# Kernel tuning notes

Hardware: AMD Instinct MI355X
Metric: run time of the kernel (lower is better)

The kernel has to match this reference:

```python
import jax, jax.numpy as jnp
import numpy as np

DIM = 2048
NUM_HEADS = 16
HEAD_DIM = DIM // NUM_HEADS
ROPE_BASE = 10000.0


def _rope_cache(seq_len):
    inv_freq = 1.0 / (ROPE_BASE ** (jnp.arange(0, HEAD_DIM, 2, dtype=jnp.float32) / HEAD_DIM))
    t = jnp.arange(seq_len, dtype=jnp.float32)
    freqs = jnp.einsum('i,j->ij', t, inv_freq)          # [S, HEAD_DIM//2]
    emb = jnp.concatenate([freqs, freqs], axis=-1)       # [S, HEAD_DIM]
    return jnp.cos(emb), jnp.sin(emb)


def _rotate_half(x):
    x1, x2 = jnp.split(x, 2, axis=-1)
    return jnp.concatenate([-x2, x1], axis=-1)


def setup_inputs() -> dict:
    key = jax.random.key(0)
    kx, kq, ko = jax.random.split(key, 3)
    B, S = 2, 2048
    x = jax.random.normal(kx, (B, S, DIM), dtype=jnp.float32)
    # torch nn.Linear(dim, 3*dim) weight has shape [3*dim, dim]; y = x @ W.T
    w_qkv = jax.random.normal(kq, (3 * DIM, DIM), dtype=jnp.float32) * (DIM ** -0.5)
    w_out = jax.random.normal(ko, (DIM, DIM), dtype=jnp.float32) * (DIM ** -0.5)
    return {"x": x, "w_qkv": w_qkv, "w_out": w_out}


def reference(x, w_qkv, w_out):
    B, S, _ = x.shape
    qkv = x @ w_qkv.T                                   # [B, S, 3*DIM]
    q, k, v = jnp.split(qkv, 3, axis=-1)
    def to_heads(t):
        return t.reshape(B, S, NUM_HEADS, HEAD_DIM).transpose(0, 2, 1, 3)  # [B, H, S, d]
    q, k, v = to_heads(q), to_heads(k), to_heads(v)

    cos, sin = _rope_cache(S)                           # [S, d]
    cos = cos[None, None, :, :]
    sin = sin[None, None, :, :]
    q = q * cos + _rotate_half(q) * sin
    k = k * cos + _rotate_half(k) * sin

    scale = HEAD_DIM ** -0.5
    scores = jnp.einsum('bhqd,bhkd->bhqk', q, k) * scale  # [B, H, S, S]
    causal = jnp.tril(jnp.ones((S, S), dtype=bool))
    scores = jnp.where(causal[None, None], scores, -jnp.inf)
    attn = jax.nn.softmax(scores, axis=-1)
    out = jnp.einsum('bhqk,bhkd->bhqd', attn, v)          # [B, H, S, d]
    out = out.transpose(0, 2, 1, 3).reshape(B, S, DIM)
    return out @ w_out.T
```

## Files before the change

### kernel.cpp

```cpp
#include <hip/hip_runtime.h>
#include <cstdint>
#include <cstddef>

#define NHEADS 16
#define HDIM   128
#define BATCH  2
#define SEQ    2048
#define DMODEL 2048
#define MTOT   (BATCH*SEQ)
#define NQKV   (3*DMODEL)
#define QBLK   64

typedef __attribute__((ext_vector_type(8))) __bf16 bf16x8;
typedef __attribute__((ext_vector_type(4))) float f32x4;
typedef __attribute__((ext_vector_type(8))) unsigned short ushort8v;

__device__ __forceinline__ unsigned short f2bf(float f){
  __bf16 h = (__bf16)f;
  return __builtin_bit_cast(unsigned short, h);
}
__device__ __forceinline__ float bf2f(unsigned short s){
  return __uint_as_float(((uint32_t)s) << 16);
}
__device__ __forceinline__ void gload_lds16(const void* src, void* lds_base){
  __builtin_amdgcn_global_load_lds((const __attribute__((address_space(1))) unsigned int*)src,
                                   (__attribute__((address_space(3))) unsigned int*)lds_base,
                                   16, 0, 0);
}

template<int CTRL>
__device__ __forceinline__ float dppmv(float x){
  return __uint_as_float((unsigned)__builtin_amdgcn_update_dpp(
      0, (int)__float_as_uint(x), CTRL, 0xF, 0xF, true));
}
__device__ __forceinline__ float rmax16(float x){
  x = fmaxf(x, dppmv<0x128>(x));
  x = fmaxf(x, dppmv<0x124>(x));
  x = fmaxf(x, dppmv<0x122>(x));
  x = fmaxf(x, dppmv<0x121>(x));
  return x;
}
__device__ __forceinline__ float rsum16(float x){
  x += dppmv<0x128>(x);
  x += dppmv<0x124>(x);
  x += dppmv<0x122>(x);
  x += dppmv<0x121>(x);
  return x;
}

__global__ void cast3_kernel(const float* __restrict__ s0, unsigned short* __restrict__ d0, int n0,
                             const float* __restrict__ s1, unsigned short* __restrict__ d1, int n1,
                             const float* __restrict__ s2, unsigned short* __restrict__ d2, int n2){
  const int stride = gridDim.x*blockDim.x*8;
  const int base = (blockIdx.x*blockDim.x + threadIdx.x)*8;
  #pragma unroll 1
  for (int a = 0; a < 3; ++a){
    const float* s = a==0 ? s0 : (a==1 ? s1 : s2);
    unsigned short* d = a==0 ? d0 : (a==1 ? d1 : d2);
    const int n = a==0 ? n0 : (a==1 ? n1 : n2);
    for (int i = base; i < n; i += stride){
      float4 x = *reinterpret_cast<const float4*>(s + i);
      float4 y = *reinterpret_cast<const float4*>(s + i + 4);
      ushort8v o;
      o[0]=f2bf(x.x); o[1]=f2bf(x.y); o[2]=f2bf(x.z); o[3]=f2bf(x.w);
      o[4]=f2bf(y.x); o[5]=f2bf(y.y); o[6]=f2bf(y.z); o[7]=f2bf(y.w);
      *reinterpret_cast<ushort8v*>(d + i) = o;
    }
  }
}

template<int MODE>
__global__ __launch_bounds__(512, 2) void gemm2(
    const unsigned short* __restrict__ A,
    const unsigned short* __restrict__ Bw,
    float* __restrict__ Cf,
    unsigned short* __restrict__ qo,
    unsigned short* __restrict__ ko,
    unsigned short* __restrict__ vo,
    int M, int N, int K)
{
  __shared__ __align__(16) unsigned short smem[49152];
  auto lds = reinterpret_cast<unsigned short (*)[3][128*64]>(smem);

  const int lane = threadIdx.x & 63;
  const int wid  = threadIdx.x >> 6;
  const int wm = wid >> 2, wn = wid & 3;
  const int hi = lane >> 4;
  const int l15 = lane & 15;

  const int nwg = gridDim.x * gridDim.y;
  const int bid = blockIdx.y * gridDim.x + blockIdx.x;
  const int swz = (bid & 7) * (nwg >> 3) + (bid >> 3);
  const int by = swz & 31;
  const int bx = swz >> 5;
  const int m0 = by * 128;
  const int n0 = bx * 256;

  const int NT = K >> 6;

  auto stage = [&](const unsigned short* base, int row0, int k0, int buf, int slot){
    const int rlo = wid << 4;
    #pragma unroll
    for (int i=0;i<2;++i){
      const int r = rlo + i*8 + (lane>>3);
      const int csrc = ((lane&7) ^ (lane>>3)) << 3;
      gload_lds16(base + (size_t)(row0 + r)*K + k0 + csrc,
                  &lds[buf][slot][(rlo + i*8)*64]);
    }
  };
  auto frag = [&](const unsigned short* h, int r, int s){
    return *reinterpret_cast<const bf16x8*>(h + r*64 + ((s ^ (r&7)) << 3));
  };

  f32x4 acc[4][4];
  #pragma unroll
  for (int i=0;i<4;++i)
    #pragma unroll
    for (int j=0;j<4;++j) acc[i][j] = (f32x4){0.f,0.f,0.f,0.f};

  stage(A,  m0,      0, 0, 0);
  stage(Bw, n0,      0, 0, 1);
  stage(Bw, n0+128,  0, 0, 2);
  if (NT > 1){
    stage(A, m0, 64, 1, 0);
    asm volatile("s_waitcnt vmcnt(2)" ::: "memory");
  } else {
    asm volatile("s_waitcnt vmcnt(0)" ::: "memory");
  }
  __builtin_amdgcn_sched_barrier(0);
  __builtin_amdgcn_s_barrier();

  bf16x8 Ar[4][2];
  bf16x8 Br[2][2];

  auto tile_body = [&](int kt, int cur){
    const int nxt = cur ^ 1;
    const unsigned short* Ah = &lds[cur][0][0];
    const unsigned short* Bh = &lds[cur][1 + (wn>>1)][0];
    const int rbase = (wn & 1) * 64;

    #pragma unroll
    for (int fm=0;fm<4;++fm)
      #pragma unroll
      for (int kk=0;kk<2;++kk)
        Ar[fm][kk] = frag(Ah, wm*64 + fm*16 + l15, kk*4 + hi);
    #pragma unroll
    for (int nf=0;nf<2;++nf)
      #pragma unroll
      for (int kk=0;kk<2;++kk)
        Br[nf][kk] = frag(Bh, rbase + nf*16 + l15, kk*4 + hi);
    if (kt+1 < NT){
      stage(Bw, n0,     (kt+1)*64, nxt, 1);
      stage(Bw, n0+128, (kt+1)*64, nxt, 2);
    }
    asm volatile("s_waitcnt lgkmcnt(8)" ::: "memory");
    __builtin_amdgcn_sched_barrier(0);
    __builtin_amdgcn_s_barrier();
    asm volatile("s_waitcnt lgkmcnt(0)" ::: "memory");
    __builtin_amdgcn_sched_barrier(0);
    __builtin_amdgcn_s_setprio(1);
    #pragma unroll
    for (int fm=0;fm<4;++fm){
      acc[fm][0] = __builtin_amdgcn_mfma_f32_16x16x32_bf16(Ar[fm][0], Br[0][0], acc[fm][0], 0,0,0);
      acc[fm][0] = __builtin_amdgcn_mfma_f32_16x16x32_bf16(Ar[fm][1], Br[0][1], acc[fm][0], 0,0,0);
      acc[fm][1] = __builtin_amdgcn_mfma_f32_16x16x32_bf16(Ar[fm][0], Br[1][0], acc[fm][1], 0,0,0);
      acc[fm][1] = __builtin_amdgcn_mfma_f32_16x16x32_bf16(Ar[fm][1], Br[1][1], acc[fm][1], 0,0,0);
    }
    __builtin_amdgcn_s_setprio(0);
    __builtin_amdgcn_sched_barrier(0);
    __builtin_amdgcn_s_barrier();

    #pragma unroll
    for (int nf=0;nf<2;++nf)
      #pragma unroll
      for (int kk=0;kk<2;++kk)
        Br[nf][kk] = frag(Bh, rbase + 32 + nf*16 + l15, kk*4 + hi);
    if (kt+2 < NT) stage(A, m0, (kt+2)*64, cur, 0);
    __builtin_amdgcn_sched_barrier(0);
    __builtin_amdgcn_s_barrier();
    asm volatile("s_waitcnt lgkmcnt(0)" ::: "memory");
    __builtin_amdgcn_sched_barrier(0);
    __builtin_amdgcn_s_setprio(1);
    #pragma unroll
    for (int fm=0;fm<4;++fm){
      acc[fm][2] = __builtin_amdgcn_mfma_f32_16x16x32_bf16(Ar[fm][0], Br[0][0], acc[fm][2], 0,0,0);
      acc[fm][2] = __builtin_amdgcn_mfma_f32_16x16x32_bf16(Ar[fm][1], Br[0][1], acc[fm][2], 0,0,0);
      acc[fm][3] = __builtin_amdgcn_mfma_f32_16x16x32_bf16(Ar[fm][0], Br[1][0], acc[fm][3], 0,0,0);
      acc[fm][3] = __builtin_amdgcn_mfma_f32_16x16x32_bf16(Ar[fm][1], Br[1][1], acc[fm][3], 0,0,0);
    }
    __builtin_amdgcn_s_setprio(0);
    if (kt+2 < NT)      asm volatile("s_waitcnt vmcnt(2)" ::: "memory");
    else if (kt+1 < NT) asm volatile("s_waitcnt vmcnt(0)" ::: "memory");
    __builtin_amdgcn_sched_barrier(0);
    __builtin_amdgcn_s_barrier();
  };

  for (int kt2 = 0; kt2 < NT; kt2 += 2){
    tile_body(kt2,     0);
    tile_body(kt2 + 1, 1);
  }

  if (MODE == 0 && (n0 >> 11) == 2){
    __builtin_amdgcn_s_barrier();
    unsigned short* trsp = smem;
    #pragma unroll
    for (int fm=0;fm<4;++fm){
      const int srow = wm*64 + fm*16 + hi*4;
      #pragma unroll
      for (int p=0;p<4;++p){
        const int dcol = wn*64 + p*16 + l15;
        f32x4 v = acc[fm][p];
        ushort4 pk;
        pk.x=f2bf(v[0]); pk.y=f2bf(v[1]); pk.z=f2bf(v[2]); pk.w=f2bf(v[3]);
        *reinterpret_cast<ushort4*>(trsp + dcol*136 + srow) = pk;
      }
    }
    __syncthreads();
    const int bb  = m0 >> 11;
    const int ss0 = m0 & 2047;
    const size_t vrow = (size_t)(bb*2048 + (n0 - 4096));
    const int t = threadIdx.x;
    #pragma unroll
    for (int it=0; it<8; ++it){
      const int dl = it*32 + (t>>4);
      const int ch = t & 15;
      ushort8v val = *reinterpret_cast<const ushort8v*>(trsp + dl*136 + ch*8);
      *reinterpret_cast<ushort8v*>(vo + (vrow + dl)*SEQ + ss0 + ch*8) = val;
    }
  } else {
    #pragma unroll
    for (int fm=0;fm<4;++fm){
      const int row0 = m0 + wm*64 + fm*16 + (hi<<2);
      #pragma unroll
      for (int p=0;p<4;++p){
        const int col = n0 + wn*64 + p*16 + l15;
        f32x4 v = acc[fm][p];
        if (MODE == 1){
          #pragma unroll
          for (int r=0;r<4;++r) Cf[(size_t)(row0+r)*N + col] = v[r];
        } else {
          const int part = col >> 11;
          const int hh = (col >> 7) & 15;
          const int d  = col & 127;
          const int bb = row0 >> 11;
          const int ss = row0 & 2047;
          unsigned short* base = (part == 0 ? qo : ko)
                               + ((size_t)(bb*NHEADS+hh)*SEQ + ss)*HDIM + d;
          #pragma unroll
          for (int r=0;r<4;++r) base[r*HDIM] = f2bf(v[r]);
        }
      }
    }
  }
}

__global__ void rope_kernel(unsigned short* __restrict__ qh, unsigned short* __restrict__ kh){
  const int idx = blockIdx.x * blockDim.x + threadIdx.x;
  const int j  = idx & 63;
  const int s  = (idx >> 6) & 2047;
  const int bh = (idx >> 17) & 31;
  const int t  = idx >> 22;
  unsigned short* base = (t ? kh : qh) + ((size_t)bh*SEQ + s)*HDIM;
  const float x1 = bf2f(base[j]);
  const float x2 = bf2f(base[j+64]);
  const float inv = exp2f(-(float)j * (13.287712379549449f/64.f));
  const float ang = (float)s * inv;
  float sn, cs;
  sincosf(ang, &sn, &cs);
  float o1 = x1*cs - x2*sn;
  float o2 = x2*cs + x1*sn;
  const float QSCALE = 0.08838834764831845f * 1.4426950408889634f;
  if (t == 0){ o1 *= QSCALE; o2 *= QSCALE; }
  base[j]    = f2bf(o1);
  base[j+64] = f2bf(o2);
}

__global__ __launch_bounds__(256, 2) void attn_kernel(
    const unsigned short* __restrict__ qh,
    const unsigned short* __restrict__ kh,
    const unsigned short* __restrict__ vT,
    unsigned short* __restrict__ ao)
{
  __shared__ __align__(16) unsigned short Ks[2][64*128];
  __shared__ __align__(16) unsigned short Vs[2][128*64];
  __shared__ __align__(16) unsigned short Ps[4][16*64];

  const int lane = threadIdx.x & 63;
  const int wid  = threadIdx.x >> 6;
  const int hi   = lane >> 4;
  const int pr = blockIdx.x;
  const int bh = blockIdx.y;
  const int b_ = bh >> 4, h_ = bh & 15;

  const unsigned short* Qb = qh + (size_t)bh * SEQ * HDIM;
  const unsigned short* Kb = kh + (size_t)bh * SEQ * HDIM;
  const unsigned short* Vb = vT + (size_t)bh * HDIM * SEQ;

  auto stageKV = [&](int kg, int buf){
    #pragma unroll
    for (int i=0;i<4;++i){
      const int r  = (wid*4+i)*4 + (lane>>4);
      const int cb = ((lane&15)<<4) ^ ((r&7)<<4);
      gload_lds16(Kb + (size_t)(kg*64 + r)*HDIM + (cb>>1), &Ks[buf][0] + (wid*4+i)*512);
    }
    #pragma unroll
    for (int i=0;i<4;++i){
      const int d  = (wid*4+i)*8 + (lane>>3);
      const int cb = ((lane&7)<<4) ^ ((d&7)<<4);
      gload_lds16(Vb + (size_t)d*SEQ + kg*64 + (cb>>1), &Vs[buf][0] + (wid*4+i)*512);
    }
  };

  for (int ph = 0; ph < 2; ++ph){
    const int qt = ph ? (31 - pr) : pr;
    const int qrow0w = qt*QBLK + wid*16;

    bf16x8 qf[4];
    {
      const int qr = qrow0w + (lane & 15);
      #pragma unroll
      for (int ks = 0; ks < 4; ++ks)
        qf[ks] = *reinterpret_cast<const bf16x8*>(Qb + (size_t)qr*HDIM + ks*32 + hi*8);
    }

    f32x4 oacc[8];
    #pragma unroll
    for (int t=0;t<8;++t) oacc[t] = (f32x4){0.f,0.f,0.f,0.f};
    float mrun[4] = {-3.0e38f,-3.0e38f,-3.0e38f,-3.0e38f};
    float lrun[4] = {0.f,0.f,0.f,0.f};

    const int nkt = qt + 1;

    stageKV(0, 0);
    __syncthreads();

    for (int kt = 0; kt < nkt; ++kt){
      const int cur = kt & 1;
      if (kt + 1 < nkt) stageKV(kt + 1, cur ^ 1);

      if (kt*64 <= qrow0w + 15){
        f32x4 sacc[4];
        #pragma unroll
        for (int nt=0;nt<4;++nt) sacc[nt] = (f32x4){0.f,0.f,0.f,0.f};
        __builtin_amdgcn_s_setprio(1);
        #pragma unroll
        for (int nt=0;nt<4;++nt){
          const int krow = nt*16 + (lane&15);
          #pragma unroll
          for (int ks=0;ks<4;++ks){
            const int cb = (ks*64 + (hi<<4)) ^ ((krow&7)<<4);
            bf16x8 kf = *reinterpret_cast<const bf16x8*>(&Ks[cur][0] + krow*128 + (cb>>1));
            sacc[nt] = __builtin_amdgcn_mfma_f32_16x16x32_bf16(qf[ks], kf, sacc[nt], 0,0,0);
          }
        }
        __builtin_amdgcn_s_setprio(0);

        if (kt*64 + 63 > qrow0w){
          #pragma unroll
          for (int nt=0;nt<4;++nt){
            const int key = kt*64 + nt*16 + (lane&15);
            #pragma unroll
            for (int r=0;r<4;++r){
              const int qr = qrow0w + hi*4 + r;
              if (key > qr) sacc[nt][r] = -1.0e30f;
            }
          }
        }

        float fac[4];
        #pragma unroll
        for (int r=0;r<4;++r){
          float mx = fmaxf(fmaxf(sacc[0][r], sacc[1][r]),
                           fmaxf(sacc[2][r], sacc[3][r]));
          mx = rmax16(mx);
          const float mnew = fmaxf(mrun[r], mx);
          fac[r] = exp2f(mrun[r] - mnew);
          mrun[r] = mnew;
          float ps = 0.f;
          #pragma unroll
          for (int nt=0;nt<4;++nt){
            const float p = exp2f(sacc[nt][r] - mnew);
            sacc[nt][r] = p;
            ps += p;
          }
          ps = rsum16(ps);
          lrun[r] = lrun[r]*fac[r] + ps;
        }
        #pragma unroll
        for (int t=0;t<8;++t)
          #pragma unroll
          for (int r=0;r<4;++r) oacc[t][r] *= fac[r];

        char* pb = (char*)&Ps[wid][0];
        #pragma unroll
        for (int nt=0;nt<4;++nt){
          const int keyb = (nt*16 + (lane&15)) << 1;
          #pragma unroll
          for (int r=0;r<4;++r){
            const int prow = hi*4 + r;
            *(unsigned short*)(pb + prow*128 + (keyb ^ ((prow&7)<<4))) = f2bf(sacc[nt][r]);
          }
        }
        asm volatile("s_waitcnt lgkmcnt(0)" ::: "memory");
        __builtin_amdgcn_sched_barrier(0);

        bf16x8 pa[2];
        {
          const int prow = lane & 15;
          #pragma unroll
          for (int ks=0;ks<2;++ks){
            const int pcb = (ks*64 + (hi<<4)) ^ ((prow&7)<<4);
            pa[ks] = *reinterpret_cast<const bf16x8*>(pb + prow*128 + pcb);
          }
        }
        __builtin_amdgcn_s_setprio(1);
        #pragma unroll
        for (int ks=0;ks<2;++ks){
          #pragma unroll
          for (int t=0;t<8;++t){
            const int drow = t*16 + (lane&15);
            const int vcb = (ks*64 + (hi<<4)) ^ ((drow&7)<<4);
            bf16x8 vb = *reinterpret_cast<const bf16x8*>(&Vs[cur][0] + drow*64 + (vcb>>1));
            oacc[t] = __builtin_amdgcn_mfma_f32_16x16x32_bf16(pa[ks], vb, oacc[t], 0,0,0);
          }
        }
        __builtin_amdgcn_s_setprio(0);
      }

      __syncthreads();
    }

    float linv[4];
    #pragma unroll
    for (int r=0;r<4;++r) linv[r] = 1.0f / lrun[r];
    #pragma unroll
    for (int t=0;t<8;++t){
      const int col = h_*HDIM + t*16 + (lane&15);
      #pragma unroll
      for (int r=0;r<4;++r){
        const int s_ = qrow0w + hi*4 + r;
        ao[(size_t)(b_*SEQ + s_)*DMODEL + col] = f2bf(oacc[t][r] * linv[r]);
      }
    }
  }
}

extern "C" void kernel_launch(void* const* d_in, const int* in_sizes, int n_in,
                              void* d_out, int out_size, void* d_ws, size_t ws_size,
                              hipStream_t stream)
{
  const float* x     = (const float*)d_in[0];
  const float* w_qkv = (const float*)d_in[1];
  const float* w_out = (const float*)d_in[2];
  float* out = (float*)d_out;

  unsigned short* xb    = (unsigned short*)d_ws;
  unsigned short* wqkvb = xb    + (size_t)MTOT*DMODEL;
  unsigned short* woutb = wqkvb + (size_t)NQKV*DMODEL;
  unsigned short* qhb   = woutb + (size_t)DMODEL*DMODEL;
  unsigned short* khb   = qhb   + (size_t)MTOT*DMODEL;
  unsigned short* vtb   = khb   + (size_t)MTOT*DMODEL;
  unsigned short* aob   = vtb   + (size_t)MTOT*DMODEL;

  hipLaunchKernelGGL(cast3_kernel, dim3(1024), dim3(256), 0, stream,
                     x, xb, MTOT*DMODEL, w_qkv, wqkvb, NQKV*DMODEL, w_out, woutb, DMODEL*DMODEL);
  hipLaunchKernelGGL((gemm2<0>), dim3(NQKV/256, MTOT/128), dim3(512), 0, stream,
                     xb, wqkvb, (float*)nullptr, qhb, khb, vtb, MTOT, NQKV, DMODEL);
  hipLaunchKernelGGL(rope_kernel, dim3((2*BATCH*NHEADS*SEQ*64)/256), dim3(256), 0, stream, qhb, khb);
  hipLaunchKernelGGL(attn_kernel, dim3(16, BATCH*NHEADS), dim3(256), 0, stream, qhb, khb, vtb, aob);
  hipLaunchKernelGGL((gemm2<1>), dim3(DMODEL/256, MTOT/128), dim3(512), 0, stream,
                     aob, woutb, out, (unsigned short*)nullptr, (unsigned short*)nullptr,
                     (unsigned short*)nullptr, MTOT, DMODEL, DMODEL);
}
```

Before: 268.7 us.

## Enlarge attention query tile to 128 rows with two fragments per wave

The attention kernel processes 128 query rows per block, with each wave owning two 16-row fragments. Each K and V fragment read from LDS then feeds two MFMAs, and each K/V tile staged from global memory serves twice as many queries. The grid halves and launch bounds drop to one block per CU. This trades occupancy and register pressure for data reuse, and with fewer blocks it risks load imbalance in the causal tail.

```diff
diff --git a/kernel.cpp b/kernel.cpp
--- a/kernel.cpp
+++ b/kernel.cpp
@@ -9,7 +9,6 @@
 #define DMODEL 2048
 #define MTOT   (BATCH*SEQ)
 #define NQKV   (3*DMODEL)
-#define QBLK   64
 
 typedef __attribute__((ext_vector_type(8))) __bf16 bf16x8;
 typedef __attribute__((ext_vector_type(4))) float f32x4;
@@ -275,7 +274,7 @@
   base[j+64] = f2bf(o2);
 }
 
-__global__ __launch_bounds__(256, 2) void attn_kernel(
+__global__ __launch_bounds__(256, 1) void attn_kernel(
     const unsigned short* __restrict__ qh,
     const unsigned short* __restrict__ kh,
     const unsigned short* __restrict__ vT,
@@ -283,11 +282,12 @@
 {
   __shared__ __align__(16) unsigned short Ks[2][64*128];
   __shared__ __align__(16) unsigned short Vs[2][128*64];
-  __shared__ __align__(16) unsigned short Ps[4][16*64];
+  __shared__ __align__(16) unsigned short Ps[4][32*64];
 
   const int lane = threadIdx.x & 63;
   const int wid  = threadIdx.x >> 6;
   const int hi   = lane >> 4;
+  const int l15  = lane & 15;
   const int pr = blockIdx.x;
   const int bh = blockIdx.y;
   const int b_ = bh >> 4, h_ = bh & 15;
@@ -312,24 +312,30 @@
   };
 
   for (int ph = 0; ph < 2; ++ph){
-    const int qt = ph ? (31 - pr) : pr;
-    const int qrow0w = qt*QBLK + wid*16;
-
-    bf16x8 qf[4];
-    {
-      const int qr = qrow0w + (lane & 15);
+    const int qt = ph ? (15 - pr) : pr;
+    const int qrow0w = qt*128 + wid*32;
+
+    bf16x8 qf[2][4];
+    #pragma unroll
+    for (int fi=0; fi<2; ++fi){
+      const int qr = qrow0w + fi*16 + l15;
       #pragma unroll
       for (int ks = 0; ks < 4; ++ks)
-        qf[ks] = *reinterpret_cast<const bf16x8*>(Qb + (size_t)qr*HDIM + ks*32 + hi*8);
-    }
-
-    f32x4 oacc[8];
-    #pragma unroll
-    for (int t=0;t<8;++t) oacc[t] = (f32x4){0.f,0.f,0.f,0.f};
-    float mrun[4] = {-3.0e38f,-3.0e38f,-3.0e38f,-3.0e38f};
-    float lrun[4] = {0.f,0.f,0.f,0.f};
-
-    const int nkt = qt + 1;
+        qf[fi][ks] = *reinterpret_cast<const bf16x8*>(Qb + (size_t)qr*HDIM + ks*32 + hi*8);
+    }
+
+    f32x4 oacc[2][8];
+    #pragma unroll
+    for (int fi=0;fi<2;++fi)
+      #pragma unroll
+      for (int t=0;t<8;++t) oacc[fi][t] = (f32x4){0.f,0.f,0.f,0.f};
+    float mrun[2][4], lrun[2][4];
+    #pragma unroll
+    for (int fi=0;fi<2;++fi)
+      #pragma unroll
+      for (int r=0;r<4;++r){ mrun[fi][r] = -3.0e38f; lrun[fi][r] = 0.f; }
+
+    const int nkt = 2*qt + 2;
 
     stageKV(0, 0);
     __syncthreads();
@@ -338,79 +344,92 @@
       const int cur = kt & 1;
       if (kt + 1 < nkt) stageKV(kt + 1, cur ^ 1);
 
-      if (kt*64 <= qrow0w + 15){
-        f32x4 sacc[4];
-        #pragma unroll
-        for (int nt=0;nt<4;++nt) sacc[nt] = (f32x4){0.f,0.f,0.f,0.f};
+      if (kt*64 <= qrow0w + 31){
+        f32x4 sacc[2][4];
+        #pragma unroll
+        for (int fi=0;fi<2;++fi)
+          #pragma unroll
+          for (int nt=0;nt<4;++nt) sacc[fi][nt] = (f32x4){0.f,0.f,0.f,0.f};
         __builtin_amdgcn_s_setprio(1);
         #pragma unroll
         for (int nt=0;nt<4;++nt){
-          const int krow = nt*16 + (lane&15);
+          const int krow = nt*16 + l15;
+          bf16x8 kf[4];
           #pragma unroll
           for (int ks=0;ks<4;++ks){
             const int cb = (ks*64 + (hi<<4)) ^ ((krow&7)<<4);
-            bf16x8 kf = *reinterpret_cast<const bf16x8*>(&Ks[cur][0] + krow*128 + (cb>>1));
-            sacc[nt] = __builtin_amdgcn_mfma_f32_16x16x32_bf16(qf[ks], kf, sacc[nt], 0,0,0);
-          }
+            kf[ks] = *reinterpret_cast<const bf16x8*>(&Ks[cur][0] + krow*128 + (cb>>1));
+          }
+          #pragma unroll
+          for (int fi=0;fi<2;++fi)
+            #pragma unroll
+            for (int ks=0;ks<4;++ks)
+              sacc[fi][nt] = __builtin_amdgcn_mfma_f32_16x16x32_bf16(qf[fi][ks], kf[ks], sacc[fi][nt], 0,0,0);
         }
         __builtin_amdgcn_s_setprio(0);
 
-        if (kt*64 + 63 > qrow0w){
+        #pragma unroll
+        for (int fi=0;fi<2;++fi){
+          if (kt*64 + 63 > qrow0w + fi*16){
+            #pragma unroll
+            for (int nt=0;nt<4;++nt){
+              const int key = kt*64 + nt*16 + l15;
+              #pragma unroll
+              for (int r=0;r<4;++r){
+                const int qr = qrow0w + fi*16 + hi*4 + r;
+                if (key > qr) sacc[fi][nt][r] = -1.0e30f;
+              }
+            }
+          }
+        }
+
+        char* pb = (char*)&Ps[wid][0];
+        #pragma unroll
+        for (int fi=0;fi<2;++fi){
+          float fac[4];
+          #pragma unroll
+          for (int r=0;r<4;++r){
+            float mx = fmaxf(fmaxf(sacc[fi][0][r], sacc[fi][1][r]),
+                             fmaxf(sacc[fi][2][r], sacc[fi][3][r]));
+            mx = rmax16(mx);
+            const float mnew = fmaxf(mrun[fi][r], mx);
+            fac[r] = exp2f(mrun[fi][r] - mnew);
+            mrun[fi][r] = mnew;
+            float ps = 0.f;
+            #pragma unroll
+            for (int nt=0;nt<4;++nt){
+              const float p = exp2f(sacc[fi][nt][r] - mnew);
+              sacc[fi][nt][r] = p;
+              ps += p;
+            }
+            ps = rsum16(ps);
+            lrun[fi][r] = lrun[fi][r]*fac[r] + ps;
+          }
+          #pragma unroll
+          for (int t=0;t<8;++t)
+            #pragma unroll
+            for (int r=0;r<4;++r) oacc[fi][t][r] *= fac[r];
           #pragma unroll
           for (int nt=0;nt<4;++nt){
-            const int key = kt*64 + nt*16 + (lane&15);
+            const int keyb = (nt*16 + l15) << 1;
             #pragma unroll
             for (int r=0;r<4;++r){
-              const int qr = qrow0w + hi*4 + r;
-              if (key > qr) sacc[nt][r] = -1.0e30f;
+              const int prow = fi*16 + hi*4 + r;
+              *(unsigned short*)(pb + prow*128 + (keyb ^ ((prow&7)<<4))) = f2bf(sacc[fi][nt][r]);
             }
-          }
-        }
-
-        float fac[4];
-        #pragma unroll
-        for (int r=0;r<4;++r){
-          float mx = fmaxf(fmaxf(sacc[0][r], sacc[1][r]),
-                           fmaxf(sacc[2][r], sacc[3][r]));
-          mx = rmax16(mx);
-          const float mnew = fmaxf(mrun[r], mx);
-          fac[r] = exp2f(mrun[r] - mnew);
-          mrun[r] = mnew;
-          float ps = 0.f;
-          #pragma unroll
-          for (int nt=0;nt<4;++nt){
-            const float p = exp2f(sacc[nt][r] - mnew);
-            sacc[nt][r] = p;
-            ps += p;
-          }
-          ps = rsum16(ps);
-          lrun[r] = lrun[r]*fac[r] + ps;
-        }
-        #pragma unroll
-        for (int t=0;t<8;++t)
-          #pragma unroll
-          for (int r=0;r<4;++r) oacc[t][r] *= fac[r];
-
-        char* pb = (char*)&Ps[wid][0];
-        #pragma unroll
-        for (int nt=0;nt<4;++nt){
-          const int keyb = (nt*16 + (lane&15)) << 1;
-          #pragma unroll
-          for (int r=0;r<4;++r){
-            const int prow = hi*4 + r;
-            *(unsigned short*)(pb + prow*128 + (keyb ^ ((prow&7)<<4))) = f2bf(sacc[nt][r]);
           }
         }
         asm volatile("s_waitcnt lgkmcnt(0)" ::: "memory");
         __builtin_amdgcn_sched_barrier(0);
 
-        bf16x8 pa[2];
-        {
-          const int prow = lane & 15;
+        bf16x8 pa[2][2];
+        #pragma unroll
+        for (int fi=0;fi<2;++fi){
+          const int prow = fi*16 + l15;
           #pragma unroll
           for (int ks=0;ks<2;++ks){
             const int pcb = (ks*64 + (hi<<4)) ^ ((prow&7)<<4);
-            pa[ks] = *reinterpret_cast<const bf16x8*>(pb + prow*128 + pcb);
+            pa[fi][ks] = *reinterpret_cast<const bf16x8*>(pb + prow*128 + pcb);
           }
         }
         __builtin_amdgcn_s_setprio(1);
@@ -418,10 +437,12 @@
         for (int ks=0;ks<2;++ks){
           #pragma unroll
           for (int t=0;t<8;++t){
-            const int drow = t*16 + (lane&15);
+            const int drow = t*16 + l15;
             const int vcb = (ks*64 + (hi<<4)) ^ ((drow&7)<<4);
             bf16x8 vb = *reinterpret_cast<const bf16x8*>(&Vs[cur][0] + drow*64 + (vcb>>1));
-            oacc[t] = __builtin_amdgcn_mfma_f32_16x16x32_bf16(pa[ks], vb, oacc[t], 0,0,0);
+            #pragma unroll
+            for (int fi=0;fi<2;++fi)
+              oacc[fi][t] = __builtin_amdgcn_mfma_f32_16x16x32_bf16(pa[fi][ks], vb, oacc[fi][t], 0,0,0);
           }
         }
         __builtin_amdgcn_s_setprio(0);
@@ -430,16 +451,19 @@
       __syncthreads();
     }
 
-    float linv[4];
-    #pragma unroll
-    for (int r=0;r<4;++r) linv[r] = 1.0f / lrun[r];
-    #pragma unroll
-    for (int t=0;t<8;++t){
-      const int col = h_*HDIM + t*16 + (lane&15);
-      #pragma unroll
-      for (int r=0;r<4;++r){
-        const int s_ = qrow0w + hi*4 + r;
-        ao[(size_t)(b_*SEQ + s_)*DMODEL + col] = f2bf(oacc[t][r] * linv[r]);
+    #pragma unroll
+    for (int fi=0;fi<2;++fi){
+      float linv[4];
+      #pragma unroll
+      for (int r=0;r<4;++r) linv[r] = 1.0f / lrun[fi][r];
+      #pragma unroll
+      for (int t=0;t<8;++t){
+        const int col = h_*HDIM + t*16 + l15;
+        #pragma unroll
+        for (int r=0;r<4;++r){
+          const int s_ = qrow0w + fi*16 + hi*4 + r;
+          ao[(size_t)(b_*SEQ + s_)*DMODEL + col] = f2bf(oacc[fi][t][r] * linv[r]);
+        }
       }
     }
   }
@@ -467,7 +491,7 @@
   hipLaunchKernelGGL((gemm2<0>), dim3(NQKV/256, MTOT/128), dim3(512), 0, stream,
                      xb, wqkvb, (float*)nullptr, qhb, khb, vtb, MTOT, NQKV, DMODEL);
   hipLaunchKernelGGL(rope_kernel, dim3((2*BATCH*NHEADS*SEQ*64)/256), dim3(256), 0, stream, qhb, khb);
-  hipLaunchKernelGGL(attn_kernel, dim3(16, BATCH*NHEADS), dim3(256), 0, stream, qhb, khb, vtb, aob);
+  hipLaunchKernelGGL(attn_kernel, dim3(8, BATCH*NHEADS), dim3(256), 0, stream, qhb, khb, vtb, aob);
   hipLaunchKernelGGL((gemm2<1>), dim3(DMODEL/256, MTOT/128), dim3(512), 0, stream,
                      aob, woutb, out, (unsigned short*)nullptr, (unsigned short*)nullptr,
                      (unsigned short*)nullptr, MTOT, DMODEL, DMODEL);
```

Measured after the change: 296.7 us. 1.1x slower.
